# Optimization experiments

Hardware: AMD Instinct MI355X
Metric: run time of the kernel (lower is better)

The kernel has to match this reference:

```python
import jax, jax.numpy as jnp
import numpy as np

B, S, D, H = 2, 2048, 1024, 16
HD = D // H  # head_dim = 64
NEG_INF = -jnp.inf


def _rope_tables(seq_len, head_dim, theta=10000.0):
    inv = 1.0 / (theta ** (np.arange(0, head_dim, 2, dtype=np.float32) / head_dim))
    t = np.arange(seq_len, dtype=np.float32)
    ang = np.outer(t, inv)  # [S, HD/2]
    return jnp.asarray(np.cos(ang)), jnp.asarray(np.sin(ang))


def _apply_rope(x, cos, sin):
    # x: [B, S, H, HD]; pairs (even, odd) rotated by complex freqs, matching
    # torch.view_as_complex(reshape(..., -1, 2)) * freqs_cis.
    x2 = x.reshape(*x.shape[:-1], HD // 2, 2)
    x0, x1 = x2[..., 0], x2[..., 1]
    c = cos[None, :, None, :]
    s = sin[None, :, None, :]
    o0 = x0 * c - x1 * s
    o1 = x0 * s + x1 * c
    return jnp.stack([o0, o1], axis=-1).reshape(x.shape)


def setup_inputs() -> dict:
    key = jax.random.key(0)
    ks = jax.random.split(key, 10)
    sc = 1.0 / np.sqrt(D)
    return {
        "x": jax.random.normal(ks[0], (B, S, D), dtype=jnp.float32),
        "effective_len": jax.random.randint(ks[1], (B,), 0, 1024, dtype=jnp.int32),
        "Wq": jax.random.normal(ks[2], (D, D), dtype=jnp.float32) * sc,
        "bq": jnp.zeros((D,), dtype=jnp.float32),
        "Wk": jax.random.normal(ks[3], (D, D), dtype=jnp.float32) * sc,
        "bk": jnp.zeros((D,), dtype=jnp.float32),
        "Wv": jax.random.normal(ks[4], (D, D), dtype=jnp.float32) * sc,
        "bv": jnp.zeros((D,), dtype=jnp.float32),
        "Wo": jax.random.normal(ks[5], (D, D), dtype=jnp.float32) * sc,
        "bo": jnp.zeros((D,), dtype=jnp.float32),
    }


def reference(x, effective_len, Wq, bq, Wk, bk, Wv, bv, Wo, bo):
    cos, sin = _rope_tables(S, HD)
    q = (x @ Wq.T + bq).reshape(B, S, H, HD)
    k = (x @ Wk.T + bk).reshape(B, S, H, HD)
    v = (x @ Wv.T + bv).reshape(B, S, H, HD)
    q = _apply_rope(q, cos, sin)
    k = _apply_rope(k, cos, sin)
    # [B, H, S, S]
    scores = jnp.einsum("bqhd,bkhd->bhqk", q, k) / np.sqrt(HD)
    row = jnp.arange(S)[:, None]
    col = jnp.arange(S)[None, :]
    causal = jnp.where(col > row, NEG_INF, 0.0)  # [S, S]
    scores = scores + causal[None, None, :, :]
    # faithful replication of original: masks the LAST effective_len key columns
    pad = jnp.where(col[None, 0, :] >= (S - effective_len)[:, None], NEG_INF, 0.0)  # [B, S]
    scores = scores + pad[:, None, None, :]
    probs = jax.nn.softmax(scores.astype(jnp.float32), axis=-1).astype(x.dtype)
    out = jnp.einsum("bhqk,bkhd->bqhd", probs, v).reshape(B, S, D)
    return out @ Wo.T + bo  # dropout in eval mode = identity
```

## Files before the change

### kernel.cpp

```cpp
#include <hip/hip_runtime.h>

#define SB   2048
#define DD   1024
#define NH   16
#define HDIM 64
#define NB   2

typedef float f4 __attribute__((ext_vector_type(4)));
typedef __bf16 bf16x8 __attribute__((ext_vector_type(8)));
typedef unsigned short u16;
typedef unsigned int u32;
typedef unsigned long long u64;
typedef u16 u16x8 __attribute__((ext_vector_type(8)));
typedef u16 u16x4 __attribute__((ext_vector_type(4)));

#define QSCALE 0.1803368801111f

__device__ __forceinline__ u16 f2bf(float f) {
  unsigned u = __float_as_uint(f);
  u += 0x7FFFu + ((u >> 16) & 1u);
  return (u16)(u >> 16);
}

typedef __attribute__((address_space(3))) unsigned int lds_uint;
typedef __attribute__((address_space(1))) const unsigned int glb_uint;
__device__ __forceinline__ void gl_lds16(const void* g, void* l) {
  __builtin_amdgcn_global_load_lds((glb_uint*)g, (lds_uint*)l, 16, 0, 0);
}

__device__ __forceinline__ void cvt8(const float* __restrict__ src,
                                     u16* __restrict__ dst, size_t i) {
  f4 a = *(const f4*)(src + 8 * i);
  f4 b = *(const f4*)(src + 8 * i + 4);
  u16x8 o;
  o[0] = f2bf(a[0]); o[1] = f2bf(a[1]); o[2] = f2bf(a[2]); o[3] = f2bf(a[3]);
  o[4] = f2bf(b[0]); o[5] = f2bf(b[1]); o[6] = f2bf(b[2]); o[7] = f2bf(b[3]);
  *(u16x8*)(dst + 8 * i) = o;
}

__global__ __launch_bounds__(256) void prep_kernel(
    const float* __restrict__ x, const float* __restrict__ Wq,
    const float* __restrict__ Wk, const float* __restrict__ Wv,
    const float* __restrict__ Wo,
    u16* __restrict__ xb, u16* __restrict__ Wb3, u16* __restrict__ WoB,
    float* __restrict__ cosT, float* __restrict__ sinT, int nwo) {
  int bid = blockIdx.x, t = threadIdx.x;
  if (bid < 2048) {
    cvt8(x, xb, (size_t)bid * 256 + t);
  } else if (bid < 2560) {
    cvt8(Wq, Wb3, (size_t)(bid - 2048) * 256 + t);
  } else if (bid < 3072) {
    cvt8(Wk, Wb3 + (1u << 20), (size_t)(bid - 2560) * 256 + t);
  } else if (bid < 3584) {
    cvt8(Wv, Wb3 + (2u << 20), (size_t)(bid - 3072) * 256 + t);
  } else if (bid < 3584 + nwo) {
    cvt8(Wo, WoB, (size_t)(bid - 3584) * 256 + t);
  } else {
    int idx = (bid - 3584 - nwo) * 256 + t;
    int tt = idx & 31, s = idx >> 5;
    float inv = powf(10000.0f, -2.0f * (float)tt / 64.0f);
    float ang = (float)s * inv;
    cosT[idx] = cosf(ang);
    sinT[idx] = sinf(ang);
  }
}

__global__ __launch_bounds__(256) void cvt_bf16_kernel(const float* __restrict__ src,
                                                       u16* __restrict__ dst) {
  cvt8(src, dst, (size_t)blockIdx.x * 256 + threadIdx.x);
}

__global__ __launch_bounds__(256, 4) void gemm_qkv_fused_kernel(
    const u16* __restrict__ A, const u16* __restrict__ W3,
    const float* __restrict__ bq, const float* __restrict__ bk,
    const float* __restrict__ bv,
    u16* __restrict__ Qw, u16* __restrict__ Kw, u16* __restrict__ Vt,
    const float* __restrict__ cosT, const float* __restrict__ sinT) {
  const int K = DD;
  __shared__ char smem[32768];
  u16* As = (u16*)smem;
  u16* Bs = (u16*)(smem + 16384);
  const int t = threadIdx.x;
  const int wave = t >> 6, lane = t & 63;
  const int m0 = blockIdx.x * 128, n0 = blockIdx.y * 128;
  const int mw = (wave >> 1) * 64, nw = (wave & 1) * 64;
  const int quad = lane >> 4, l15 = lane & 15;
  const int srow = lane >> 3, sgran = lane & 7;
  const u16* Ab = A + (size_t)m0 * K;
  const u16* Bb = W3 + (size_t)n0 * K;
  f4 acc[4][4];
#pragma unroll
  for (int i = 0; i < 4; i++)
#pragma unroll
    for (int j = 0; j < 4; j++) acc[i][j] = (f4)0.f;

  for (int kt = 0; kt < K; kt += 64) {
#pragma unroll
    for (int is = 0; is < 4; is++) {
      int r = wave * 32 + is * 8 + srow;
      int lg = sgran ^ (r & 7);
      gl_lds16(Ab + (size_t)r * K + kt + lg * 8, &As[(wave * 32 + is * 8) * 64]);
      gl_lds16(Bb + (size_t)r * K + kt + lg * 8, &Bs[(wave * 32 + is * 8) * 64]);
    }
    __syncthreads();
#pragma unroll
    for (int kh = 0; kh < 2; kh++) {
      bf16x8 af[4], bfr[4];
#pragma unroll
      for (int i = 0; i < 4; i++) {
        int R = mw + 16 * i + l15;
        af[i] = *(const bf16x8*)&As[R * 64 + ((kh * 4 + quad) ^ (R & 7)) * 8];
        int Rb = nw + 16 * i + l15;
        bfr[i] = *(const bf16x8*)&Bs[Rb * 64 + ((kh * 4 + quad) ^ (Rb & 7)) * 8];
      }
#pragma unroll
      for (int i = 0; i < 4; i++)
#pragma unroll
        for (int j = 0; j < 4; j++)
          acc[i][j] = __builtin_amdgcn_mfma_f32_16x16x32_bf16(af[i], bfr[j],
                                                              acc[i][j], 0, 0, 0);
    }
    __syncthreads();
  }

  const int which = n0 >> 10;
  const int hh = ((n0 & 1023) + nw) >> 6;
  const int cb = (n0 + nw) & 1023;

  if (which == 2) {
#pragma unroll
    for (int j = 0; j < 4; j++) {
      const int dh = 16 * j + l15;
      const float bval = bv[cb + 16 * j + l15];
#pragma unroll
      for (int i = 0; i < 4; i++) {
        int mg0 = m0 + mw + 16 * i + quad * 4;
        int b = mg0 >> 11, sr0 = mg0 & (SB - 1);
        u16x4 pk4;
#pragma unroll
        for (int r = 0; r < 4; r++) pk4[r] = f2bf(acc[i][j][r] + bval);
        *(u16x4*)(Vt + ((size_t)(b * NH + hh) * HDIM + dh) * SB + sr0) = pk4;
      }
    }
  } else {
    u16* dst = which ? Kw : Qw;
    const float* barr = which ? bk : bq;
    const float scale = which ? 1.0f : QSCALE;
    float bvj[4];
#pragma unroll
    for (int j = 0; j < 4; j++) bvj[j] = barr[cb + 16 * j + l15];
    float* sl = (float*)(smem + wave * 8192);
    const int kk = lane >> 1, hf = lane & 1;
#pragma unroll
    for (int half = 0; half < 2; half++) {
#pragma unroll
      for (int il = 0; il < 2; il++) {
#pragma unroll
        for (int j = 0; j < 4; j++) {
          const int q = 4 * j + (l15 >> 2);
          const int w = l15 & 3;
#pragma unroll
          for (int r = 0; r < 4; r++) {
            const int row = il * 16 + quad * 4 + r;
            sl[(row << 6) + (((q + row) & 15) << 2) + w] =
                (acc[half * 2 + il][j][r] + bvj[j]) * scale;
          }
        }
      }
      asm volatile("s_waitcnt lgkmcnt(0)" ::: "memory");
      const int m = m0 + mw + half * 32 + kk;
      const int b = m >> 11, sr = m & (SB - 1);
      const float* ct = cosT + sr * 32 + hf * 16;
      const float* st2 = sinT + sr * 32 + hf * 16;
      u16* op = dst + (((size_t)(b * NH + hh)) * SB + sr) * HDIM + hf * 32;
#pragma unroll
      for (int q8 = 0; q8 < 4; q8++) {
        f4 c4 = *(const f4*)(ct + q8 * 4);
        f4 s4 = *(const f4*)(st2 + q8 * 4);
        const int qc0 = hf * 8 + q8 * 2;
        f4 v0 = *(const f4*)(sl + (kk << 6) + (((qc0 + kk) & 15) << 2));
        f4 v1 = *(const f4*)(sl + (kk << 6) + (((qc0 + 1 + kk) & 15) << 2));
        u16x8 o;
        o[0] = f2bf(v0[0] * c4[0] - v0[1] * s4[0]);
        o[1] = f2bf(v0[0] * s4[0] + v0[1] * c4[0]);
        o[2] = f2bf(v0[2] * c4[1] - v0[3] * s4[1]);
        o[3] = f2bf(v0[2] * s4[1] + v0[3] * c4[1]);
        o[4] = f2bf(v1[0] * c4[2] - v1[1] * s4[2]);
        o[5] = f2bf(v1[0] * s4[2] + v1[1] * c4[2]);
        o[6] = f2bf(v1[2] * c4[3] - v1[3] * s4[3]);
        o[7] = f2bf(v1[2] * s4[3] + v1[3] * c4[3]);
        *(u16x8*)(op + q8 * 8) = o;
      }
      if (half == 0) asm volatile("s_waitcnt lgkmcnt(0)" ::: "memory");
    }
  }
}

__global__ __launch_bounds__(256) void gemm_out_kernel(
    const u16* __restrict__ A, const u16* __restrict__ W,
    const float* __restrict__ bias, float* __restrict__ outp) {
  const int K = DD;
  __shared__ u16 As[128 * 64];
  __shared__ u16 Bs[64 * 64];
  const int t = threadIdx.x;
  const int wave = t >> 6, lane = t & 63;
  const int m0 = blockIdx.x * 128, n0 = blockIdx.y * 64;
  const int mw = (wave >> 1) * 64, nw = (wave & 1) * 32;
  const int quad = lane >> 4, l15 = lane & 15;
  const int srow = lane >> 3, sgran = lane & 7;
  const u16* Ab = A + (size_t)m0 * K;
  const u16* Bb = W + (size_t)n0 * K;
  f4 acc[4][2];
#pragma unroll
  for (int i = 0; i < 4; i++)
#pragma unroll
    for (int j = 0; j < 2; j++) acc[i][j] = (f4)0.f;

  for (int kt = 0; kt < K; kt += 64) {
#pragma unroll
    for (int is = 0; is < 4; is++) {
      int r = wave * 32 + is * 8 + srow;
      int lg = sgran ^ (r & 7);
      gl_lds16(Ab + (size_t)r * K + kt + lg * 8, &As[(wave * 32 + is * 8) * 64]);
    }
#pragma unroll
    for (int is = 0; is < 2; is++) {
      int r = wave * 16 + is * 8 + srow;
      int lg = sgran ^ (r & 7);
      gl_lds16(Bb + (size_t)r * K + kt + lg * 8, &Bs[(wave * 16 + is * 8) * 64]);
    }
    __syncthreads();
#pragma unroll
    for (int kh = 0; kh < 2; kh++) {
      bf16x8 af[4], bfr[2];
#pragma unroll
      for (int i = 0; i < 4; i++) {
        int R = mw + 16 * i + l15;
        af[i] = *(const bf16x8*)&As[R * 64 + ((kh * 4 + quad) ^ (R & 7)) * 8];
      }
#pragma unroll
      for (int j = 0; j < 2; j++) {
        int R = nw + 16 * j + l15;
        bfr[j] = *(const bf16x8*)&Bs[R * 64 + ((kh * 4 + quad) ^ (R & 7)) * 8];
      }
#pragma unroll
      for (int i = 0; i < 4; i++)
#pragma unroll
        for (int j = 0; j < 2; j++)
          acc[i][j] = __builtin_amdgcn_mfma_f32_16x16x32_bf16(af[i], bfr[j],
                                                              acc[i][j], 0, 0, 0);
    }
    __syncthreads();
  }
#pragma unroll
  for (int i = 0; i < 4; i++)
#pragma unroll
    for (int j = 0; j < 2; j++) {
      int colg = n0 + nw + 16 * j + l15;
#pragma unroll
      for (int r = 0; r < 4; r++) {
        int mg = m0 + mw + 16 * i + quad * 4 + r;
        outp[(size_t)mg * DD + colg] = acc[i][j][r] + bias[colg];
      }
    }
}

__global__ __launch_bounds__(512) void attn_mfma_kernel(
    const u16* __restrict__ Qw, const u16* __restrict__ Kw,
    const u16* __restrict__ Vt, u16* __restrict__ Ow,
    const int* __restrict__ eff) {
  __shared__ u16 KL[2][8 * 64 * 8];
  __shared__ u16 VL[2][8 * 64 * 8];
  const int w = threadIdx.x >> 6, lane = threadIdx.x & 63;
  const int l15 = lane & 15, q4 = lane >> 4;
  const int qp = blockIdx.x;
  const int wg = w >> 2, wl = w & 3;
  const int QT = wg ? (SB / 128 - 1 - qp) : qp;
  const int h = blockIdx.y, b = blockIdx.z;
  const int limit = SB - eff[b];
  const size_t bh = ((size_t)b * NH + h) * (SB * HDIM);

  const int rowbase = QT * 128 + wl * 32;

  bf16x8 qf[2][2];
  {
    const u16* qp0 = Qw + bh + (size_t)(rowbase + l15) * HDIM + q4 * 8;
    qf[0][0] = *(const bf16x8*)qp0;
    qf[0][1] = *(const bf16x8*)(qp0 + 32);
    const u16* qp1 = qp0 + 16 * HDIM;
    qf[1][0] = *(const bf16x8*)qp1;
    qf[1][1] = *(const bf16x8*)(qp1 + 32);
  }

  f4 acc[2][4];
#pragma unroll
  for (int s = 0; s < 2; s++)
#pragma unroll
    for (int dt = 0; dt < 4; dt++) acc[s][dt] = (f4)0.f;
  float l_run[2] = {0.f, 0.f};

  const int kendB = min((SB / 128 - 1 - qp) * 128 + 127, limit - 1);
  const int ntiles = (kendB >> 6) + 1;
  const int wkend = min(rowbase + 31, limit - 1);

#define STAGE_TILE(TILE, BUF)                                                   \
  {                                                                             \
    const int colb_ = (TILE) * 64;                                              \
    _Pragma("unroll") for (int f = 0; f < 2; f++) {                             \
      int fr = w * 2 + f;                                                       \
      if (fr < 8) {                                                             \
        int mt = fr >> 1, j = fr & 1;                                           \
        gl_lds16(Kw + bh + (size_t)(colb_ + mt * 16 + l15) * HDIM + q4 * 8 + j * 32, \
                 &KL[BUF][fr * 512]);                                           \
      } else {                                                                  \
        int fv = fr - 8, dt = fv >> 1, j = fv & 1;                              \
        gl_lds16(Vt + bh + (size_t)(dt * 16 + l15) * SB + colb_ + q4 * 8 + j * 32, \
                 &VL[BUF][fv * 512]);                                           \
      }                                                                         \
    }                                                                           \
  }

  STAGE_TILE(0, 0)
  __syncthreads();

  for (int kt = 0; kt < ntiles; kt++) {
    const int cur = kt & 1;
    const int colb = kt * 64;
    if (kt + 1 < ntiles) STAGE_TILE(kt + 1, cur ^ 1)

    if (colb <= wkend) {
      f4 sa[2][4];
#pragma unroll
      for (int mt = 0; mt < 4; mt++) {
        bf16x8 k0 = *(const bf16x8*)&KL[cur][(mt * 2 + 0) * 512 + lane * 8];
        bf16x8 k1 = *(const bf16x8*)&KL[cur][(mt * 2 + 1) * 512 + lane * 8];
        f4 s0 = (f4)0.f, s1 = (f4)0.f;
        s0 = __builtin_amdgcn_mfma_f32_16x16x32_bf16(k0, qf[0][0], s0, 0, 0, 0);
        s0 = __builtin_amdgcn_mfma_f32_16x16x32_bf16(k1, qf[0][1], s0, 0, 0, 0);
        s1 = __builtin_amdgcn_mfma_f32_16x16x32_bf16(k0, qf[1][0], s1, 0, 0, 0);
        s1 = __builtin_amdgcn_mfma_f32_16x16x32_bf16(k1, qf[1][1], s1, 0, 0, 0);
        sa[0][mt] = s0;
        sa[1][mt] = s1;
      }

      u32 pk[2][4][2];
#pragma unroll
      for (int s = 0; s < 2; s++) {
        const int rb = rowbase + 16 * s;
        const int rg = rb + l15;
        const bool needmask = (colb + 63 > rb) || (colb + 63 >= limit);
        if (needmask) {
#pragma unroll
          for (int mt = 0; mt < 4; mt++)
#pragma unroll
            for (int r = 0; r < 4; r++) {
              int col = colb + mt * 16 + q4 * 4 + r;
              if (col > rg || col >= limit) sa[s][mt][r] = -3.0e38f;
            }
        }
        float lsum = 0.f;
#pragma unroll
        for (int mt = 0; mt < 4; mt++) {
          float p0 = exp2f(sa[s][mt][0]);
          float p1 = exp2f(sa[s][mt][1]);
          float p2 = exp2f(sa[s][mt][2]);
          float p3 = exp2f(sa[s][mt][3]);
          lsum += (p0 + p1) + (p2 + p3);
          pk[s][mt][0] = (__float_as_uint(p1) & 0xFFFF0000u) | (__float_as_uint(p0) >> 16);
          pk[s][mt][1] = (__float_as_uint(p3) & 0xFFFF0000u) | (__float_as_uint(p2) >> 16);
        }
        l_run[s] += lsum;
      }

      const int srcA = ((q4 & 1) << 5) + l15;
      const int hi = q4 >> 1;
#pragma unroll
      for (int s = 0; s < 2; s++) {
        union { u32 wds[4]; bf16x8 v; } ub0, ub1;
#pragma unroll
        for (int d = 0; d < 4; d++) {
          int src = srcA + ((d >> 1) << 4);
          u32 t0 = (u32)__shfl((int)pk[s][0][d & 1], src);
          u32 t1 = (u32)__shfl((int)pk[s][1][d & 1], src);
          ub0.wds[d] = hi ? t1 : t0;
          u32 t2 = (u32)__shfl((int)pk[s][2][d & 1], src);
          u32 t3 = (u32)__shfl((int)pk[s][3][d & 1], src);
          ub1.wds[d] = hi ? t3 : t2;
        }
#pragma unroll
        for (int dt = 0; dt < 4; dt++) {
          bf16x8 v0 = *(const bf16x8*)&VL[cur][(dt * 2 + 0) * 512 + lane * 8];
          bf16x8 v1 = *(const bf16x8*)&VL[cur][(dt * 2 + 1) * 512 + lane * 8];
          acc[s][dt] = __builtin_amdgcn_mfma_f32_16x16x32_bf16(v0, ub0.v, acc[s][dt], 0, 0, 0);
          acc[s][dt] = __builtin_amdgcn_mfma_f32_16x16x32_bf16(v1, ub1.v, acc[s][dt], 0, 0, 0);
        }
      }
    }
    __syncthreads();
  }

#pragma unroll
  for (int s = 0; s < 2; s++) {
    float lt = l_run[s];
    lt += __shfl_xor(lt, 16);
    lt += __shfl_xor(lt, 32);
    const float linv = 1.0f / lt;
    const int rg = rowbase + 16 * s + l15;
    const size_t obase = (((size_t)b * SB + rg) * NH + h) * HDIM + q4 * 4;
#pragma unroll
    for (int dt = 0; dt < 4; dt++) {
      u16x4 o;
      o[0] = f2bf(acc[s][dt][0] * linv);
      o[1] = f2bf(acc[s][dt][1] * linv);
      o[2] = f2bf(acc[s][dt][2] * linv);
      o[3] = f2bf(acc[s][dt][3] * linv);
      *(u16x4*)(Ow + obase + dt * 16) = o;
    }
  }
}

extern "C" void kernel_launch(void* const* d_in, const int* in_sizes, int n_in,
                              void* d_out, int out_size, void* d_ws, size_t ws_size,
                              hipStream_t stream) {
  (void)in_sizes; (void)n_in; (void)out_size;
  const float* x  = (const float*)d_in[0];
  const int*   eff = (const int*)d_in[1];
  const float* Wq = (const float*)d_in[2];
  const float* bq = (const float*)d_in[3];
  const float* Wk = (const float*)d_in[4];
  const float* bk = (const float*)d_in[5];
  const float* Wv = (const float*)d_in[6];
  const float* bv = (const float*)d_in[7];
  const float* Wo = (const float*)d_in[8];
  const float* bo = (const float*)d_in[9];
  float* out = (float*)d_out;

  char* ws = (char*)d_ws;
  u16* Qw = (u16*)(ws);
  u16* Kw = (u16*)(ws + (8u << 20));
  u16* Vt = (u16*)(ws + (16u << 20));
  u16* Ow = (u16*)(ws + (24u << 20));
  u16* xb = (u16*)(ws + (24u << 20));
  u16* Wb3 = (u16*)(ws + (32u << 20));
  float* cosT = (float*)(ws + (38u << 20));
  float* sinT = (float*)(ws + (38u << 20) + (256u << 10));

  size_t wob_off = (38u << 20) + (512u << 10);
  int nwo = (ws_size >= wob_off + (2u << 20)) ? 512 : 0;
  u16* WoB = nwo ? (u16*)(ws + wob_off) : Wb3;

  hipLaunchKernelGGL(prep_kernel, dim3(3840 + nwo), dim3(256), 0, stream,
                     x, Wq, Wk, Wv, Wo, xb, Wb3, WoB, cosT, sinT, nwo);

  hipLaunchKernelGGL(gemm_qkv_fused_kernel, dim3(32, 24), dim3(256), 0, stream,
                     xb, Wb3, bq, bk, bv, Qw, Kw, Vt, cosT, sinT);

  if (!nwo)
    hipLaunchKernelGGL(cvt_bf16_kernel, dim3(512), dim3(256), 0, stream, Wo, WoB);

  hipLaunchKernelGGL(attn_mfma_kernel, dim3(SB / 256, NH, NB), dim3(512), 0, stream,
                     Qw, Kw, Vt, Ow, eff);

  hipLaunchKernelGGL(gemm_out_kernel, dim3(32, 16), dim3(256), 0, stream, Ow, WoB, bo, out);
}
```

Baseline: 202.1 us.

## Permute V layout to drop P shuffles, flatten attn grid, add MFMA priority

```diff
diff --git a/kernel.cpp b/kernel.cpp
--- a/kernel.cpp
+++ b/kernel.cpp
@@ -136,10 +136,11 @@
       for (int i = 0; i < 4; i++) {
         int mg0 = m0 + mw + 16 * i + quad * 4;
         int b = mg0 >> 11, sr0 = mg0 & (SB - 1);
+        int sp0 = (sr0 & ~31) | (quad << 3) | ((i & 1) << 2);
         u16x4 pk4;
 #pragma unroll
         for (int r = 0; r < 4; r++) pk4[r] = f2bf(acc[i][j][r] + bval);
-        *(u16x4*)(Vt + ((size_t)(b * NH + hh) * HDIM + dh) * SB + sr0) = pk4;
+        *(u16x4*)(Vt + ((size_t)(b * NH + hh) * HDIM + dh) * SB + sp0) = pk4;
       }
     }
   } else {
@@ -273,10 +274,12 @@
   __shared__ u16 VL[2][8 * 64 * 8];
   const int w = threadIdx.x >> 6, lane = threadIdx.x & 63;
   const int l15 = lane & 15, q4 = lane >> 4;
-  const int qp = blockIdx.x;
+  const int lid = blockIdx.x;
+  const int qp = lid >> 5;
+  const int c  = lid & 31;
+  const int h = c & 15, b = c >> 4;
   const int wg = w >> 2, wl = w & 3;
   const int QT = wg ? (SB / 128 - 1 - qp) : qp;
-  const int h = blockIdx.y, b = blockIdx.z;
   const int limit = SB - eff[b];
   const size_t bh = ((size_t)b * NH + h) * (SB * HDIM);
 
@@ -330,6 +333,7 @@
 
     if (colb <= wkend) {
       f4 sa[2][4];
+      __builtin_amdgcn_s_setprio(1);
 #pragma unroll
       for (int mt = 0; mt < 4; mt++) {
         bf16x8 k0 = *(const bf16x8*)&KL[cur][(mt * 2 + 0) * 512 + lane * 8];
@@ -342,6 +346,7 @@
         sa[0][mt] = s0;
         sa[1][mt] = s1;
       }
+      __builtin_amdgcn_s_setprio(0);
 
       u32 pk[2][4][2];
 #pragma unroll
@@ -372,21 +377,14 @@
         l_run[s] += lsum;
       }
 
-      const int srcA = ((q4 & 1) << 5) + l15;
-      const int hi = q4 >> 1;
+      __builtin_amdgcn_s_setprio(1);
 #pragma unroll
       for (int s = 0; s < 2; s++) {
         union { u32 wds[4]; bf16x8 v; } ub0, ub1;
-#pragma unroll
-        for (int d = 0; d < 4; d++) {
-          int src = srcA + ((d >> 1) << 4);
-          u32 t0 = (u32)__shfl((int)pk[s][0][d & 1], src);
-          u32 t1 = (u32)__shfl((int)pk[s][1][d & 1], src);
-          ub0.wds[d] = hi ? t1 : t0;
-          u32 t2 = (u32)__shfl((int)pk[s][2][d & 1], src);
-          u32 t3 = (u32)__shfl((int)pk[s][3][d & 1], src);
-          ub1.wds[d] = hi ? t3 : t2;
-        }
+        ub0.wds[0] = pk[s][0][0]; ub0.wds[1] = pk[s][0][1];
+        ub0.wds[2] = pk[s][1][0]; ub0.wds[3] = pk[s][1][1];
+        ub1.wds[0] = pk[s][2][0]; ub1.wds[1] = pk[s][2][1];
+        ub1.wds[2] = pk[s][3][0]; ub1.wds[3] = pk[s][3][1];
 #pragma unroll
         for (int dt = 0; dt < 4; dt++) {
           bf16x8 v0 = *(const bf16x8*)&VL[cur][(dt * 2 + 0) * 512 + lane * 8];
@@ -395,6 +393,7 @@
           acc[s][dt] = __builtin_amdgcn_mfma_f32_16x16x32_bf16(v1, ub1.v, acc[s][dt], 0, 0, 0);
         }
       }
+      __builtin_amdgcn_s_setprio(0);
     }
     __syncthreads();
   }
@@ -458,7 +457,7 @@
   if (!nwo)
     hipLaunchKernelGGL(cvt_bf16_kernel, dim3(512), dim3(256), 0, stream, Wo, WoB);
 
-  hipLaunchKernelGGL(attn_mfma_kernel, dim3(SB / 256, NH, NB), dim3(512), 0, stream,
+  hipLaunchKernelGGL(attn_mfma_kernel, dim3(256), dim3(512), 0, stream,
                      Qw, Kw, Vt, Ow, eff);
 
   hipLaunchKernelGGL(gemm_out_kernel, dim3(32, 16), dim3(256), 0, stream, Ow, WoB, bo, out);
```

New measurement: 198.7 us. Within noise of the previous version (-1.7%).
